# Performance work log

Hardware: AMD Instinct MI355X
Metric: run time of the kernel (lower is better)

## Reference

```python
import jax, jax.numpy as jnp
import numpy as np

B = 16384
INPUT_DIM = 2048
HIDDEN = 1536
N_COMP = 256
N_LAYERS = 32
TOP_K = 4


def setup_inputs() -> dict:
    key = jax.random.key(0)
    ks = jax.random.split(key, 12)
    s_in = 1.0 / np.sqrt(INPUT_DIM)
    s_h = 1.0 / np.sqrt(HIDDEN)
    s_3 = 1.0 / np.sqrt(3)
    return {
        "x": jax.random.normal(ks[0], (B, INPUT_DIM), dtype=jnp.float32),
        "layer_idx": 3,
        "embed": jax.random.normal(ks[1], (N_LAYERS, INPUT_DIM), dtype=jnp.float32),
        "enc_w1": jax.random.uniform(ks[2], (INPUT_DIM, HIDDEN), jnp.float32, -s_in, s_in),
        "enc_b1": jax.random.uniform(ks[3], (HIDDEN,), jnp.float32, -s_in, s_in),
        "enc_w2": jax.random.uniform(ks[4], (HIDDEN, N_COMP), jnp.float32, -s_h, s_h),
        "enc_b2": jax.random.uniform(ks[5], (N_COMP,), jnp.float32, -s_h, s_h),
        "components": jax.random.normal(ks[6], (N_COMP, 3), dtype=jnp.float32),
        "dec_w1": jax.random.uniform(ks[7], (3, HIDDEN), jnp.float32, -s_3, s_3),
        "dec_b1": jax.random.uniform(ks[8], (HIDDEN,), jnp.float32, -s_3, s_3),
        "dec_w2": jax.random.uniform(ks[9], (HIDDEN, INPUT_DIM), jnp.float32, -s_h, s_h),
        "dec_b2": jax.random.uniform(ks[10], (INPUT_DIM,), jnp.float32, -s_h, s_h),
    }


def reference(x, layer_idx, embed, enc_w1, enc_b1, enc_w2, enc_b2,
              components, dec_w1, dec_b1, dec_w2, dec_b2):
    # x: (B, D). Add per-layer embedding row.
    x = x + embed[layer_idx]
    # Encoder MLP: Linear -> GELU (exact, erf-based like torch default) -> Linear
    h = jax.nn.gelu(x @ enc_w1 + enc_b1, approximate=False)
    logits = h @ enc_w2 + enc_b2                     # (B, C)
    # Top-k gated masked softmax: softmax over only the top_k logits per row.
    vals, idx = jax.lax.top_k(logits, TOP_K)         # (B, K), (B, K)
    w = jax.nn.softmax(vals, axis=-1)                # (B, K)
    # Sparse mix: equivalent to masked_fill(-inf) softmax @ components
    pts = jnp.einsum('bk,bkc->bc', w, components[idx])  # (B, 3)
    # Decoder MLP
    d = jax.nn.gelu(pts @ dec_w1 + dec_b1, approximate=False)
    decoded = d @ dec_w2 + dec_b2                    # (B, D)
    encoded = jnp.broadcast_to(components[None], (x.shape[0], N_COMP, 3))
    return encoded, decoded
```

## Files before the change

### kernel.cpp

```cpp
#include <hip/hip_runtime.h>


typedef float  f32x4  __attribute__((ext_vector_type(4)));
typedef short  short8 __attribute__((ext_vector_type(8)));
typedef int    i32x4  __attribute__((ext_vector_type(4)));

#define DEVINL __device__ __forceinline__

constexpr int  NB      = 16384;
constexpr int  IN_DIM  = 2048;
constexpr int  HID     = 1536;
constexpr int  NC      = 256;
constexpr long ENC_ELEMS = (long)NB * NC * 3;
constexpr float TAU  = 2e-5f;
constexpr float TAU1 = 1.5e-3f;
constexpr int  MAXR  = 64;
constexpr int  M2CAP = 4096;
constexpr int  NKT1 = IN_DIM / 32;
constexpr int  NKT2 = HID / 32;

constexpr float SCALE_X  = 3251.2f;
constexpr float SCALE_W1 = 1471325.0f;
constexpr float SCALE_H  = 4644.5714f;
constexpr float SCALE_W2 = 1274205.0f;
constexpr double INV_S1 = 1.0 / ((double)SCALE_X * (double)SCALE_W1);
constexpr double INV_S2 = 1.0 / ((double)SCALE_H * (double)SCALE_W2);

DEVINL unsigned short f2bf(float f) {
  unsigned int u = __builtin_bit_cast(unsigned int, f);
  u = u + 0x7fffu + ((u >> 16) & 1u);
  return (unsigned short)(u >> 16);
}
DEVINL float bf2f(unsigned short h) {
  unsigned int u = ((unsigned int)h) << 16;
  return __builtin_bit_cast(float, u);
}
DEVINL float gelu_f(float v) {
  return 0.5f * v * (1.0f + erff(v * 0.70710678118654752440f));
}
DEVINL void llds16(const void* g, void* l) {
  __builtin_amdgcn_global_load_lds(
      (const __attribute__((address_space(1))) void*)g,
      (__attribute__((address_space(3))) void*)l, 16, 0, 0);
}
DEVINL f32x4 mfma_bf16(short8 a, short8 b, f32x4 c) {
  return __builtin_amdgcn_mfma_f32_16x16x32_bf16(a, b, c, 0, 0, 0);
}
DEVINL i32x4 mfma_i8(i32x4 a, i32x4 b, i32x4 c) {
  return __builtin_amdgcn_mfma_i32_16x16x64_i8(a, b, c, 0, 0, 0);
}
DEVINL long packed_off(long tileIdx, int rowp, int kq, int e) {
  int slot = kq ^ ((rowp >> 1) & 3);
  return (tileIdx * 512 + rowp * 4 + slot) * 8 + e;
}
DEVINL int swz_idx(int rowp, int kq) {
  return (rowp * 4 + (kq ^ ((rowp >> 1) & 3))) * 8;
}
DEVINL long i8_off(long tile64, int rowp, int kin64) {
  return tile64 * 8192 + rowp * 64 + kin64;
}
DEVINL int quant16(float v, float scale) {
  int q = (int)lrintf(v * scale);
  if (q >  32512) q =  32512;
  if (q < -32512) q = -32512;
  return q;
}

__global__ __launch_bounds__(256) void transpose_split_kernel(
    const float* __restrict__ in, int K, int N, int nkt,
    unsigned short* __restrict__ outH, unsigned short* __restrict__ outL)
{
  __shared__ float t[32][33];
  int tx = threadIdx.x & 31, ty = threadIdx.x >> 5;
  int n0 = blockIdx.x * 32, k0 = blockIdx.y * 32;
#pragma unroll
  for (int i = 0; i < 4; ++i)
    t[ty + i * 8][tx] = in[(long)(k0 + ty + i * 8) * N + n0 + tx];
  __syncthreads();

  int n = n0 + tx;
  int ntile = n >> 7, rowp = n & 127;
  int Kt = k0 >> 5;
  int j = ty & 3;
  long off = packed_off((long)ntile * nkt + Kt, rowp, j, 0);
  if (ty < 4) {
    short8 hv;
#pragma unroll
    for (int e = 0; e < 8; ++e) hv[e] = (short)f2bf(t[j * 8 + e][tx]);
    *(short8*)(outH + off) = hv;
  } else if (outL) {
    short8 lv;
#pragma unroll
    for (int e = 0; e < 8; ++e) {
      float f = t[j * 8 + e][tx];
      lv[e] = (short)f2bf(f - bf2f(f2bf(f)));
    }
    *(short8*)(outL + off) = lv;
  }
}

__global__ __launch_bounds__(256) void transpose_quant_kernel(
    const float* __restrict__ in, int K, int N, int nkt64, float scale,
    char* __restrict__ outH, char* __restrict__ outL)
{
  __shared__ float t[32][33];
  int tx = threadIdx.x & 31, ty = threadIdx.x >> 5;
  int n0 = blockIdx.x * 32, k0 = blockIdx.y * 32;
#pragma unroll
  for (int i = 0; i < 4; ++i)
    t[ty + i * 8][tx] = in[(long)(k0 + ty + i * 8) * N + n0 + tx];
  __syncthreads();

  int n = n0 + tx;
  int j = ty & 3;
  int kb = k0 + j * 8;
  long off = i8_off((long)(n >> 7) * nkt64 + (kb >> 6), n & 127, kb & 63);
  union { char b[8]; long v; } u;
  if (ty < 4) {
#pragma unroll
    for (int e = 0; e < 8; ++e) {
      int q = quant16(t[j * 8 + e][tx], scale);
      int lo = (q << 24) >> 24;
      u.b[e] = (char)((q - lo) >> 8);
    }
    *(long*)(outH + off) = u.v;
  } else {
#pragma unroll
    for (int e = 0; e < 8; ++e) {
      int q = quant16(t[j * 8 + e][tx], scale);
      u.b[e] = (char)((q << 24) >> 24);
    }
    *(long*)(outL + off) = u.v;
  }
}

__global__ __launch_bounds__(256) void quant_x_kernel(
    const float* __restrict__ x, const float* __restrict__ embedMat,
    const int* __restrict__ liPtr, char* __restrict__ Xh, char* __restrict__ Xl,
    int* __restrict__ cnt, int* __restrict__ cnt2)
{
  if (blockIdx.x == 0 && threadIdx.x == 0) { *cnt = 0; *cnt2 = 0; }
  long g = (long)blockIdx.x * 256 + threadIdx.x;
  int row = (int)(g >> 7);
  int k0 = ((int)(g & 127)) * 16;
  int li = liPtr[0];
  const float* xr = x + (long)row * IN_DIM + k0;
  const float* er = embedMat + (long)li * IN_DIM + k0;
  union { char b[16]; i32x4 v; } hu, lu;
#pragma unroll
  for (int c = 0; c < 4; ++c) {
    f32x4 a = *(const f32x4*)(xr + c * 4);
    f32x4 e = *(const f32x4*)(er + c * 4);
#pragma unroll
    for (int jj = 0; jj < 4; ++jj) {
      int q = quant16(a[jj] + e[jj], SCALE_X);
      int lo = (q << 24) >> 24;
      hu.b[c * 4 + jj] = (char)((q - lo) >> 8);
      lu.b[c * 4 + jj] = (char)lo;
    }
  }
  long off = i8_off((long)(row >> 7) * (IN_DIM / 64) + (k0 >> 6), row & 127, k0 & 63);
  *(i32x4*)(Xh + off) = hu.v;
  *(i32x4*)(Xl + off) = lu.v;
}

template<int OUT>
__global__ __launch_bounds__(256, 2) void gemm_i8_kernel(
    const char* __restrict__ Ah, const char* __restrict__ Al,
    const char* __restrict__ Bh, const char* __restrict__ Bl,
    int nkt64, const float* __restrict__ bias, double invScale,
    float* __restrict__ Cf, long ldc,
    char* __restrict__ Qh, char* __restrict__ Ql, int nktOut64, float outScale,
    int nbn)
{
  __shared__ alignas(16) char sAh[8192];
  __shared__ alignas(16) char sAl[8192];
  __shared__ alignas(16) char sBh[8192];
  __shared__ alignas(16) char sBl[8192];
  __shared__ float sBias[128];

  int tid = threadIdx.x;
  int nwg = gridDim.x, q = nwg >> 3, b0 = blockIdx.x;
  int sw = (b0 & 7) * q + (b0 >> 3);
  int bm = sw / nbn, bn = sw % nbn;

  if (tid < 128) sBias[tid] = bias[bn * 128 + tid];

  int wid = tid >> 6, lane = tid & 63;
  int wm = wid >> 1, wn = wid & 1;
  int l15 = lane & 15, kq = lane >> 4;

  i32x4 accH[4][4] = {};
  i32x4 accM[4][4] = {};

  for (int kt = 0; kt < nkt64; ++kt) {
    __syncthreads();
    {
      const char* g0 = Ah + ((long)(bm * nkt64 + kt)) * 8192 + tid * 16;
      llds16(g0, sAh + tid * 16); llds16(g0 + 4096, sAh + 4096 + tid * 16);
      const char* g1 = Al + ((long)(bm * nkt64 + kt)) * 8192 + tid * 16;
      llds16(g1, sAl + tid * 16); llds16(g1 + 4096, sAl + 4096 + tid * 16);
      const char* g2 = Bh + ((long)(bn * nkt64 + kt)) * 8192 + tid * 16;
      llds16(g2, sBh + tid * 16); llds16(g2 + 4096, sBh + 4096 + tid * 16);
      const char* g3 = Bl + ((long)(bn * nkt64 + kt)) * 8192 + tid * 16;
      llds16(g3, sBl + tid * 16); llds16(g3 + 4096, sBl + 4096 + tid * 16);
    }
    __syncthreads();

    i32x4 bhf[4], blf[4];
#pragma unroll
    for (int n = 0; n < 4; ++n) {
      int off = (wn * 64 + n * 16 + l15) * 64 + kq * 16;
      bhf[n] = *(const i32x4*)&sBh[off];
      blf[n] = *(const i32x4*)&sBl[off];
    }
#pragma unroll
    for (int m = 0; m < 4; ++m) {
      int off = (wm * 64 + m * 16 + l15) * 64 + kq * 16;
      i32x4 ahf = *(const i32x4*)&sAh[off];
      i32x4 alf = *(const i32x4*)&sAl[off];
#pragma unroll
      for (int n = 0; n < 4; ++n) {
        accH[m][n] = mfma_i8(ahf, bhf[n], accH[m][n]);
        accM[m][n] = mfma_i8(alf, bhf[n], accM[m][n]);
        accM[m][n] = mfma_i8(ahf, blf[n], accM[m][n]);
      }
    }
  }

#pragma unroll
  for (int m = 0; m < 4; ++m) {
#pragma unroll
    for (int n = 0; n < 4; ++n) {
      int  gcol = bn * 128 + wn * 64 + n * 16 + l15;
      float bb  = sBias[wn * 64 + n * 16 + l15];
#pragma unroll
      for (int r = 0; r < 4; ++r) {
        long grow = (long)bm * 128 + wm * 64 + m * 16 + kq * 4 + r;
        double dv = (double)accH[m][n][r] * 65536.0 + (double)accM[m][n][r] * 256.0;
        float v = (float)(dv * invScale) + bb;
        if constexpr (OUT == 0) {
          Cf[grow * ldc + gcol] = v;
        } else {
          v = gelu_f(v);
          int qq = quant16(v, outScale);
          int lo = (qq << 24) >> 24;
          long off = i8_off((long)(grow >> 7) * nktOut64 + (gcol >> 6),
                            (int)(grow & 127), gcol & 63);
          Qh[off] = (char)((qq - lo) >> 8);
          Ql[off] = (char)lo;
        }
      }
    }
  }
}

template<bool SPLIT, int OUT_MODE, bool GELU>
__global__ __launch_bounds__(256) void gemm2_kernel(
    const unsigned short* __restrict__ Ah, const unsigned short* __restrict__ Al,
    const unsigned short* __restrict__ Bh, const unsigned short* __restrict__ Bl,
    int nkt, const float* __restrict__ bias, float* __restrict__ Cf,
    unsigned short* __restrict__ Ch, unsigned short* __restrict__ Cl,
    long ldc, int nktOut, int nbn, const int* __restrict__ mrows, int mcap)
{
  __shared__ alignas(16) unsigned short sAh[4096];
  __shared__ alignas(16) unsigned short sAl[SPLIT ? 4096 : 8];
  __shared__ alignas(16) unsigned short sBh[4096];
  __shared__ alignas(16) unsigned short sBl[SPLIT ? 4096 : 8];
  __shared__ float sBias[128];

  int tid = threadIdx.x;
  int nwg = gridDim.x, q = nwg >> 3, b0 = blockIdx.x;
  int sw = (b0 & 7) * q + (b0 >> 3);
  int bm = sw / nbn, bn = sw % nbn;

  if (mrows) {
    int v = *mrows; if (v > mcap) v = mcap;
    if (bm * 128 >= v) return;
  }

  if (tid < 128) sBias[tid] = bias[bn * 128 + tid];

  int wid = tid >> 6, lane = tid & 63;
  int wm = wid >> 1, wn = wid & 1;
  int l15 = lane & 15, kq = lane >> 4;

  f32x4 acc[4][4] = {};

  for (int kt = 0; kt < nkt; ++kt) {
    __syncthreads();
    {
      const char* gA = (const char*)Ah + ((long)(bm * nkt + kt)) * 8192 + tid * 16;
      llds16(gA,        (char*)sAh + tid * 16);
      llds16(gA + 4096, (char*)sAh + 4096 + tid * 16);
    }
    if constexpr (SPLIT) {
      const char* gA = (const char*)Al + ((long)(bm * nkt + kt)) * 8192 + tid * 16;
      llds16(gA,        (char*)sAl + tid * 16);
      llds16(gA + 4096, (char*)sAl + 4096 + tid * 16);
    }
    {
      const char* gB = (const char*)Bh + ((long)(bn * nkt + kt)) * 8192 + tid * 16;
      llds16(gB,        (char*)sBh + tid * 16);
      llds16(gB + 4096, (char*)sBh + 4096 + tid * 16);
    }
    if constexpr (SPLIT) {
      const char* gB = (const char*)Bl + ((long)(bn * nkt + kt)) * 8192 + tid * 16;
      llds16(gB,        (char*)sBl + tid * 16);
      llds16(gB + 4096, (char*)sBl + 4096 + tid * 16);
    }
    __syncthreads();

    short8 bh[4], bl[4];
#pragma unroll
    for (int n = 0; n < 4; ++n) {
      int idx = swz_idx(wn * 64 + n * 16 + l15, kq);
      bh[n] = *(const short8*)&sBh[idx];
      if constexpr (SPLIT) bl[n] = *(const short8*)&sBl[idx];
    }
#pragma unroll
    for (int m = 0; m < 4; ++m) {
      int idx = swz_idx(wm * 64 + m * 16 + l15, kq);
      short8 ah = *(const short8*)&sAh[idx];
      short8 al;
      if constexpr (SPLIT) al = *(const short8*)&sAl[idx];
#pragma unroll
      for (int n = 0; n < 4; ++n) {
        acc[m][n] = mfma_bf16(ah, bh[n], acc[m][n]);
        if constexpr (SPLIT) {
          acc[m][n] = mfma_bf16(al, bh[n], acc[m][n]);
          acc[m][n] = mfma_bf16(ah, bl[n], acc[m][n]);
        }
      }
    }
  }

#pragma unroll
  for (int m = 0; m < 4; ++m) {
#pragma unroll
    for (int n = 0; n < 4; ++n) {
      int  gcol = bn * 128 + wn * 64 + n * 16 + l15;
      float bb  = sBias[wn * 64 + n * 16 + l15];
#pragma unroll
      for (int r = 0; r < 4; ++r) {
        long grow = (long)bm * 128 + wm * 64 + m * 16 + kq * 4 + r;
        float v = acc[m][n][r] + bb;
        if constexpr (GELU) v = gelu_f(v);
        if constexpr (OUT_MODE == 0) {
          Cf[grow * ldc + gcol] = v;
        } else {
          int Mt = (int)(grow >> 7), rowpo = (int)(grow & 127);
          int Kt = gcol >> 5, kqo = (gcol >> 3) & 3, e = gcol & 7;
          long off = packed_off((long)Mt * nktOut + Kt, rowpo, kqo, e);
          unsigned short hb = f2bf(v);
          Ch[off] = hb;
          Cl[off] = f2bf(v - bf2f(hb));
        }
      }
    }
  }
}

__global__ __launch_bounds__(256) void topk_screen_kernel(
    const float* __restrict__ logits, const float* __restrict__ comp,
    float* __restrict__ pts, float* __restrict__ encOut,
    int* __restrict__ cnt2, int* __restrict__ list2,
    int* __restrict__ rescueCnt, int* __restrict__ rescueList)
{
  int wid = threadIdx.x >> 6, lane = threadIdx.x & 63;
  long row = (long)blockIdx.x * 4 + wid;
  f32x4 v4 = *(const f32x4*)(logits + row * NC + lane * 4);
  float a[4] = {v4[0], v4[1], v4[2], v4[3]};

  float tv[5]; int ti[5];
#pragma unroll
  for (int t = 0; t < 5; ++t) {
    float lv = a[0]; int li = lane * 4;
#pragma unroll
    for (int i = 1; i < 4; ++i)
      if (a[i] > lv) { lv = a[i]; li = lane * 4 + i; }
#pragma unroll
    for (int off = 32; off >= 1; off >>= 1) {
      float ov = __shfl_xor(lv, off);
      int   oi = __shfl_xor(li, off);
      if (ov > lv || (ov == lv && oi < li)) { lv = ov; li = oi; }
    }
    tv[t] = lv; ti[t] = li;
    if (t < 4 && (li >> 2) == lane) a[li & 3] = -INFINITY;
  }

  bool flag = (tv[3] - tv[4]) < TAU1;
  if (!flag) {
    float m = tv[0], w[4], s = 0.f;
#pragma unroll
    for (int t = 0; t < 4; ++t) { w[t] = expf(tv[t] - m); s += w[t]; }
    float inv = 1.0f / s;
    if (lane < 3) {
      float p = 0.f;
#pragma unroll
      for (int t = 0; t < 4; ++t) p += w[t] * inv * comp[ti[t] * 3 + lane];
      pts[row * 3 + lane] = p;
    }
  } else if (lane == 0) {
    int pos = atomicAdd(cnt2, 1);
    if (pos < M2CAP) list2[pos] = (int)row;
    else { int rp = atomicAdd(rescueCnt, 1); rescueList[rp] = (int)row; }
  }

  long base = (long)blockIdx.x * 3072;
  for (int j = threadIdx.x; j < 3072; j += 256)
    encOut[base + j] = comp[j % 768];
}

__global__ __launch_bounds__(256) void gather_kernel(
    const float* __restrict__ x, const float* __restrict__ embedMat,
    const int* __restrict__ liPtr, const int* __restrict__ cnt2,
    const int* __restrict__ list2,
    unsigned short* __restrict__ A2h, unsigned short* __restrict__ A2l)
{
  int i = blockIdx.x;
  int c2 = *cnt2; if (c2 > M2CAP) c2 = M2CAP;
  if (i >= c2) return;
  int row = list2[i];
  int li = liPtr[0];
  int t = threadIdx.x;
  int k0 = t * 8;
  const float* xr = x + (long)row * IN_DIM + k0;
  const float* er = embedMat + (long)li * IN_DIM + k0;
  short8 hv, lv;
#pragma unroll
  for (int c = 0; c < 2; ++c) {
    f32x4 a = *(const f32x4*)(xr + c * 4);
    f32x4 e = *(const f32x4*)(er + c * 4);
#pragma unroll
    for (int jj = 0; jj < 4; ++jj) {
      float f = a[jj] + e[jj];
      unsigned short hb = f2bf(f);
      hv[c * 4 + jj] = (short)hb;
      lv[c * 4 + jj] = (short)f2bf(f - bf2f(hb));
    }
  }
  long off = packed_off((long)(i >> 7) * NKT1 + (k0 >> 5), i & 127, (k0 >> 3) & 3, 0);
  *(short8*)(A2h + off) = hv;
  *(short8*)(A2l + off) = lv;
}

__global__ __launch_bounds__(256) void topk_final_kernel(
    const float* __restrict__ logits2, const float* __restrict__ comp,
    const int* __restrict__ cnt2, const int* __restrict__ list2,
    float* __restrict__ pts, int* __restrict__ rescueCnt, int* __restrict__ rescueList)
{
  int wid = threadIdx.x >> 6, lane = threadIdx.x & 63;
  int slot = blockIdx.x * 4 + wid;
  int c2 = *cnt2; if (c2 > M2CAP) c2 = M2CAP;
  if (slot >= c2) return;
  int row = list2[slot];
  f32x4 v4 = *(const f32x4*)(logits2 + (long)slot * NC + lane * 4);
  float a[4] = {v4[0], v4[1], v4[2], v4[3]};

  float tv[5]; int ti[5];
#pragma unroll
  for (int t = 0; t < 5; ++t) {
    float lv = a[0]; int li = lane * 4;
#pragma unroll
    for (int i = 1; i < 4; ++i)
      if (a[i] > lv) { lv = a[i]; li = lane * 4 + i; }
#pragma unroll
    for (int off = 32; off >= 1; off >>= 1) {
      float ov = __shfl_xor(lv, off);
      int   oi = __shfl_xor(li, off);
      if (ov > lv || (ov == lv && oi < li)) { lv = ov; li = oi; }
    }
    tv[t] = lv; ti[t] = li;
    if (t < 4 && (li >> 2) == lane) a[li & 3] = -INFINITY;
  }

  float m = tv[0], w[4], s = 0.f;
#pragma unroll
  for (int t = 0; t < 4; ++t) { w[t] = expf(tv[t] - m); s += w[t]; }
  float inv = 1.0f / s;
  if (lane < 3) {
    float p = 0.f;
#pragma unroll
    for (int t = 0; t < 4; ++t) p += w[t] * inv * comp[ti[t] * 3 + lane];
    pts[(long)row * 3 + lane] = p;
  }
  if (lane == 0 && (tv[3] - tv[4]) < TAU) {
    int pos = atomicAdd(rescueCnt, 1);
    rescueList[pos] = row;
  }
}

__global__ __launch_bounds__(256) void rescue_h1_kernel(
    const float* __restrict__ x, const float* __restrict__ embedMat,
    const int* __restrict__ liPtr, const float* __restrict__ W1,
    const int* __restrict__ cnt, const int* __restrict__ list,
    double* __restrict__ partial)
{
  int b = blockIdx.x;
  int s = b / 24, rem = b % 24;
  int cc = rem >> 2, kp = rem & 3;
  int n = *cnt;
  if (s >= n || s >= MAXR) return;
  int row = list[s];
  __shared__ double xd[512];
  int tid = threadIdx.x;
  int li = liPtr[0];
  int k0 = kp * 512;
  for (int j = tid; j < 512; j += 256)
    xd[j] = (double)x[(long)row * IN_DIM + k0 + j]
          + (double)embedMat[(long)li * IN_DIM + k0 + j];
  __syncthreads();
  int c = cc * 256 + tid;
  const float* wp = W1 + (long)k0 * HID + c;
  double s0 = 0, s1 = 0, s2 = 0, s3 = 0;
  for (int k = 0; k < 512; k += 4) {
    s0 += xd[k]     * (double)wp[(long)k * HID];
    s1 += xd[k + 1] * (double)wp[(long)(k + 1) * HID];
    s2 += xd[k + 2] * (double)wp[(long)(k + 2) * HID];
    s3 += xd[k + 3] * (double)wp[(long)(k + 3) * HID];
  }
  partial[((long)(s * 6 + cc) * 4 + kp) * 256 + tid] = (s0 + s1) + (s2 + s3);
}

__global__ __launch_bounds__(256) void rescue_h2_kernel(
    const float* __restrict__ b1, const int* __restrict__ cnt,
    const double* __restrict__ partial, double* __restrict__ hbuf)
{
  int b = blockIdx.x;
  int s = b / 6, cc = b % 6;
  int n = *cnt;
  if (s >= n || s >= MAXR) return;
  int tid = threadIdx.x;
  long base = ((long)(s * 6 + cc) * 4) * 256 + tid;
  double v = (double)b1[cc * 256 + tid]
           + ((partial[base] + partial[base + 256])
            + (partial[base + 512] + partial[base + 768]));
  hbuf[(long)s * HID + cc * 256 + tid]
      = 0.5 * v * (1.0 + erf(v * 0.70710678118654752440));
}

__global__ __launch_bounds__(256) void rescue_logits_kernel(
    const float* __restrict__ W2, const float* __restrict__ b2,
    const float* __restrict__ comp, const int* __restrict__ cnt,
    const int* __restrict__ list, const double* __restrict__ hbuf,
    float* __restrict__ pts)
{
  int s = blockIdx.x;
  int n = *cnt;
  if (s >= n || s >= MAXR) return;
  __shared__ double hd[HID];
  __shared__ double ld[NC];
  int tid = threadIdx.x;
  for (int j = tid; j < HID; j += 256) hd[j] = hbuf[(long)s * HID + j];
  __syncthreads();
  {
    const float* wp = W2 + tid;
    double a0 = 0, a1 = 0, a2 = 0, a3 = 0;
    for (int k = 0; k < HID; k += 4) {
      a0 += hd[k]     * (double)wp[(long)k * NC];
      a1 += hd[k + 1] * (double)wp[(long)(k + 1) * NC];
      a2 += hd[k + 2] * (double)wp[(long)(k + 2) * NC];
      a3 += hd[k + 3] * (double)wp[(long)(k + 3) * NC];
    }
    ld[tid] = (double)b2[tid] + ((a0 + a1) + (a2 + a3));
  }
  __syncthreads();
  if (tid == 0) {
    int row = list[s];
    int idx[4]; double val[4];
    unsigned long long mask[4] = {0, 0, 0, 0};
    for (int t = 0; t < 4; ++t) {
      double bv = -1e300; int bi = 0;
      for (int j = 0; j < NC; ++j) {
        if ((mask[j >> 6] >> (j & 63)) & 1ull) continue;
        if (ld[j] > bv) { bv = ld[j]; bi = j; }
      }
      idx[t] = bi; val[t] = bv; mask[bi >> 6] |= 1ull << (bi & 63);
    }
    double m = val[0], w[4], sum = 0;
    for (int t = 0; t < 4; ++t) { w[t] = exp(val[t] - m); sum += w[t]; }
    for (int c = 0; c < 3; ++c) {
      double p = 0;
      for (int t = 0; t < 4; ++t) p += (w[t] / sum) * (double)comp[idx[t] * 3 + c];
      pts[(long)row * 3 + c] = (float)p;
    }
  }
}

__global__ __launch_bounds__(256) void rescue_slow_kernel(
    const float* __restrict__ x, const float* __restrict__ embedMat,
    const int* __restrict__ liPtr, const float* __restrict__ W1,
    const float* __restrict__ b1, const float* __restrict__ W2,
    const float* __restrict__ b2, const float* __restrict__ comp,
    float* __restrict__ pts, const int* __restrict__ cnt, const int* __restrict__ list)
{
  __shared__ double xd[IN_DIM];
  __shared__ double hd[HID];
  __shared__ double ld[NC];
  int tid = threadIdx.x;
  int li = liPtr[0];
  int n = *cnt;
  for (int it = MAXR + blockIdx.x; it < n; it += gridDim.x) {
    int row = list[it];
    const float* xr = x + (long)row * IN_DIM;
    const float* er = embedMat + (long)li * IN_DIM;
    for (int j = tid; j < IN_DIM; j += 256)
      xd[j] = (double)xr[j] + (double)er[j];
    __syncthreads();
    for (int c = tid; c < HID; c += 256) {
      double s0 = 0, s1 = 0, s2 = 0, s3 = 0;
      const float* wp = W1 + c;
      for (int k = 0; k < IN_DIM; k += 4) {
        s0 += xd[k]     * (double)wp[(long)k * HID];
        s1 += xd[k + 1] * (double)wp[(long)(k + 1) * HID];
        s2 += xd[k + 2] * (double)wp[(long)(k + 2) * HID];
        s3 += xd[k + 3] * (double)wp[(long)(k + 3) * HID];
      }
      double s = (double)b1[c] + ((s0 + s1) + (s2 + s3));
      hd[c] = 0.5 * s * (1.0 + erf(s * 0.70710678118654752440));
    }
    __syncthreads();
    {
      int c = tid;
      double s0 = 0, s1 = 0, s2 = 0, s3 = 0;
      const float* wp = W2 + c;
      for (int k = 0; k < HID; k += 4) {
        s0 += hd[k]     * (double)wp[(long)k * NC];
        s1 += hd[k + 1] * (double)wp[(long)(k + 1) * NC];
        s2 += hd[k + 2] * (double)wp[(long)(k + 2) * NC];
        s3 += hd[k + 3] * (double)wp[(long)(k + 3) * NC];
      }
      ld[c] = (double)b2[c] + ((s0 + s1) + (s2 + s3));
    }
    __syncthreads();
    if (tid == 0) {
      int idx[4]; double val[4];
      unsigned long long mask[4] = {0, 0, 0, 0};
      for (int t = 0; t < 4; ++t) {
        double bv = -1e300; int bi = 0;
        for (int j = 0; j < NC; ++j) {
          if ((mask[j >> 6] >> (j & 63)) & 1ull) continue;
          if (ld[j] > bv) { bv = ld[j]; bi = j; }
        }
        idx[t] = bi; val[t] = bv; mask[bi >> 6] |= 1ull << (bi & 63);
      }
      double m = val[0], w[4], s = 0;
      for (int t = 0; t < 4; ++t) { w[t] = exp(val[t] - m); s += w[t]; }
      for (int c = 0; c < 3; ++c) {
        double p = 0;
        for (int t = 0; t < 4; ++t) p += (w[t] / s) * (double)comp[idx[t] * 3 + c];
        pts[(long)row * 3 + c] = (float)p;
      }
    }
    __syncthreads();
  }
}

__global__ __launch_bounds__(256) void dec_a_kernel(
    const float* __restrict__ pts, const float* __restrict__ W1d,
    const float* __restrict__ b1d, unsigned short* __restrict__ dout)
{
  int  j = (blockIdx.x % 6) * 256 + threadIdx.x;
  long b = blockIdx.x / 6;
  const float* p = pts + b * 3;
  float s = fmaf(p[0], W1d[j], fmaf(p[1], W1d[HID + j], fmaf(p[2], W1d[2 * HID + j], b1d[j])));
  int Mt = (int)(b >> 7), rowp = (int)(b & 127);
  int Kt = j >> 5, kq = (j >> 3) & 3, e = j & 7;
  dout[packed_off((long)Mt * NKT2 + Kt, rowp, kq, e)] = f2bf(gelu_f(s));
}

extern "C" void kernel_launch(void* const* d_in, const int* in_sizes, int n_in,
                              void* d_out, int out_size, void* d_ws, size_t ws_size,
                              hipStream_t stream) {
  const float* x     = (const float*)d_in[0];
  const int*   liPtr = (const int*)  d_in[1];
  const float* embed = (const float*)d_in[2];
  const float* W1    = (const float*)d_in[3];
  const float* b1    = (const float*)d_in[4];
  const float* W2    = (const float*)d_in[5];
  const float* b2    = (const float*)d_in[6];
  const float* comp  = (const float*)d_in[7];
  const float* W1d   = (const float*)d_in[8];
  const float* b1d   = (const float*)d_in[9];
  const float* W2d   = (const float*)d_in[10];
  const float* b2d   = (const float*)d_in[11];
  float* out = (float*)d_out;

  char* w = (char*)d_ws;
  unsigned short* W1hT = (unsigned short*)(w);
  unsigned short* W1lT = (unsigned short*)(w + 6291456);
  unsigned short* W2hT = (unsigned short*)(w + 12582912);
  unsigned short* W2lT = (unsigned short*)(w + 13369344);
  unsigned short* W2dT = (unsigned short*)(w + 14155776);
  char* W1qh = w + 20447232;
  char* W1ql = w + 23592960;
  char* W2qh = w + 26738688;
  char* W2ql = w + 27131904;
  char* Xqh = w + 27525120;
  char* Xql = w + 61079552;
  char* Hqh = w + 94633984;
  char* Hql = w + 119799808;
  float* logits = (float*)(w + 144965632);
  unsigned short* A2h = (unsigned short*)(w + 161742848);
  unsigned short* A2l = (unsigned short*)(w + 178520064);
  unsigned short* H2h = (unsigned short*)(w + 195297280);
  unsigned short* H2l = (unsigned short*)(w + 207880192);
  float* logits2 = (float*)(w + 220463104);
  unsigned short* dbuf = (unsigned short*)(w + 27525120);
  float* pts   = (float*)(w + 224657408);
  int*   cnt   = (int*)  (w + 224854016);
  int*   cnt2  = (int*)  (w + 224854272);
  int*   list  = (int*)  (w + 224854528);
  int*   list2 = (int*)  (w + 224920064);
  double* partial = (double*)(w + 224936448);
  double* hbuf    = (double*)(w + 228082176);

  transpose_split_kernel<<<dim3(HID / 32, IN_DIM / 32), 256, 0, stream>>>(W1, IN_DIM, HID, NKT1, W1hT, W1lT);
  transpose_split_kernel<<<dim3(NC / 32, HID / 32),     256, 0, stream>>>(W2, HID, NC, NKT2, W2hT, W2lT);
  transpose_split_kernel<<<dim3(IN_DIM / 32, HID / 32), 256, 0, stream>>>(W2d, HID, IN_DIM, NKT2, W2dT, nullptr);
  transpose_quant_kernel<<<dim3(HID / 32, IN_DIM / 32), 256, 0, stream>>>(W1, IN_DIM, HID, IN_DIM / 64, SCALE_W1, W1qh, W1ql);
  transpose_quant_kernel<<<dim3(NC / 32, HID / 32),     256, 0, stream>>>(W2, HID, NC, HID / 64, SCALE_W2, W2qh, W2ql);

  quant_x_kernel<<<NB * 128 / 256, 256, 0, stream>>>(x, embed, liPtr, Xqh, Xql, cnt, cnt2);
  gemm_i8_kernel<1><<<(NB / 128) * (HID / 128), 256, 0, stream>>>(
      Xqh, Xql, W1qh, W1ql, IN_DIM / 64, b1, INV_S1,
      nullptr, 0, Hqh, Hql, HID / 64, SCALE_H, HID / 128);
  gemm_i8_kernel<0><<<(NB / 128) * (NC / 128), 256, 0, stream>>>(
      Hqh, Hql, W2qh, W2ql, HID / 64, b2, INV_S2,
      logits, NC, nullptr, nullptr, 0, 0.f, NC / 128);

  topk_screen_kernel<<<NB / 4, 256, 0, stream>>>(logits, comp, pts, out, cnt2, list2, cnt, list);

  gather_kernel<<<M2CAP, 256, 0, stream>>>(x, embed, liPtr, cnt2, list2, A2h, A2l);
  gemm2_kernel<true, 2, true><<<(M2CAP / 128) * (HID / 128), 256, 0, stream>>>(
      A2h, A2l, W1hT, W1lT, NKT1, b1, nullptr, H2h, H2l, 0, NKT2, HID / 128, cnt2, M2CAP);
  gemm2_kernel<true, 0, false><<<(M2CAP / 128) * (NC / 128), 256, 0, stream>>>(
      H2h, H2l, W2hT, W2lT, NKT2, b2, logits2, nullptr, nullptr, NC, 0, NC / 128, cnt2, M2CAP);
  topk_final_kernel<<<M2CAP / 4, 256, 0, stream>>>(logits2, comp, cnt2, list2, pts, cnt, list);

  rescue_h1_kernel<<<MAXR * 24, 256, 0, stream>>>(x, embed, liPtr, W1, cnt, list, partial);
  rescue_h2_kernel<<<MAXR * 6,  256, 0, stream>>>(b1, cnt, partial, hbuf);
  rescue_logits_kernel<<<MAXR,  256, 0, stream>>>(W2, b2, comp, cnt, list, hbuf, pts);
  rescue_slow_kernel<<<64, 256, 0, stream>>>(x, embed, liPtr, W1, b1, W2, b2, comp, pts, cnt, list);

  dec_a_kernel<<<NB * (HID / 256), 256, 0, stream>>>(pts, W1d, b1d, dbuf);
  gemm2_kernel<false, 0, false><<<(NB / 128) * (IN_DIM / 128), 256, 0, stream>>>(
      dbuf, nullptr, W2dT, nullptr, NKT2, b2d, out + ENC_ELEMS, nullptr, nullptr,
      IN_DIM, 0, IN_DIM / 128, nullptr, 0);
}
```

Measured before the change: 753.0 us.

## Halve recompute cap, unroll K in split GEMMs, vectorize encOut, grid-stride dec_a

Four separate changes. The cap on rows sent to the precise recompute path drops from 4096 to 2048, and the split-bf16 recompute GEMMs now stage four K tiles per barrier pair instead of one. The broadcast of components into the encoded output uses 16-byte vector stores, and the decoder first layer uses a fixed 3072-block grid-stride loop instead of one block per 256 outputs. Fewer barriers and launches are the aim, but the larger shared-memory footprint (about 128KB for the split GEMM) cuts occupancy, and a smaller cap pushes more overflow rows onto the slow rescue path.

```diff
diff --git a/kernel.cpp b/kernel.cpp
--- a/kernel.cpp
+++ b/kernel.cpp
@@ -15,7 +15,7 @@
 constexpr float TAU  = 2e-5f;
 constexpr float TAU1 = 1.5e-3f;
 constexpr int  MAXR  = 64;
-constexpr int  M2CAP = 4096;
+constexpr int  M2CAP = 2048;
 constexpr int  NKT1 = IN_DIM / 32;
 constexpr int  NKT2 = HID / 32;
 
@@ -255,7 +255,7 @@
   }
 }
 
-template<bool SPLIT, int OUT_MODE, bool GELU>
+template<bool SPLIT, int OUT_MODE, bool GELU, int KU>
 __global__ __launch_bounds__(256) void gemm2_kernel(
     const unsigned short* __restrict__ Ah, const unsigned short* __restrict__ Al,
     const unsigned short* __restrict__ Bh, const unsigned short* __restrict__ Bl,
@@ -263,10 +263,10 @@
     unsigned short* __restrict__ Ch, unsigned short* __restrict__ Cl,
     long ldc, int nktOut, int nbn, const int* __restrict__ mrows, int mcap)
 {
-  __shared__ alignas(16) unsigned short sAh[4096];
-  __shared__ alignas(16) unsigned short sAl[SPLIT ? 4096 : 8];
-  __shared__ alignas(16) unsigned short sBh[4096];
-  __shared__ alignas(16) unsigned short sBl[SPLIT ? 4096 : 8];
+  __shared__ alignas(16) unsigned short sAh[4096 * KU];
+  __shared__ alignas(16) unsigned short sAl[SPLIT ? 4096 * KU : 8];
+  __shared__ alignas(16) unsigned short sBh[4096 * KU];
+  __shared__ alignas(16) unsigned short sBl[SPLIT ? 4096 * KU : 8];
   __shared__ float sBias[128];
 
   int tid = threadIdx.x;
@@ -287,49 +287,55 @@
 
   f32x4 acc[4][4] = {};
 
-  for (int kt = 0; kt < nkt; ++kt) {
+  for (int kt = 0; kt < nkt; kt += KU) {
     __syncthreads();
-    {
-      const char* gA = (const char*)Ah + ((long)(bm * nkt + kt)) * 8192 + tid * 16;
-      llds16(gA,        (char*)sAh + tid * 16);
-      llds16(gA + 4096, (char*)sAh + 4096 + tid * 16);
-    }
-    if constexpr (SPLIT) {
-      const char* gA = (const char*)Al + ((long)(bm * nkt + kt)) * 8192 + tid * 16;
-      llds16(gA,        (char*)sAl + tid * 16);
-      llds16(gA + 4096, (char*)sAl + 4096 + tid * 16);
-    }
-    {
-      const char* gB = (const char*)Bh + ((long)(bn * nkt + kt)) * 8192 + tid * 16;
-      llds16(gB,        (char*)sBh + tid * 16);
-      llds16(gB + 4096, (char*)sBh + 4096 + tid * 16);
-    }
-    if constexpr (SPLIT) {
-      const char* gB = (const char*)Bl + ((long)(bn * nkt + kt)) * 8192 + tid * 16;
-      llds16(gB,        (char*)sBl + tid * 16);
-      llds16(gB + 4096, (char*)sBl + 4096 + tid * 16);
+#pragma unroll
+    for (int u = 0; u < KU; ++u) {
+      {
+        const char* gA = (const char*)Ah + ((long)(bm * nkt + kt + u)) * 8192 + tid * 16;
+        llds16(gA,        (char*)sAh + u * 8192 + tid * 16);
+        llds16(gA + 4096, (char*)sAh + u * 8192 + 4096 + tid * 16);
+      }
+      if constexpr (SPLIT) {
+        const char* gA = (const char*)Al + ((long)(bm * nkt + kt + u)) * 8192 + tid * 16;
+        llds16(gA,        (char*)sAl + u * 8192 + tid * 16);
+        llds16(gA + 4096, (char*)sAl + u * 8192 + 4096 + tid * 16);
+      }
+      {
+        const char* gB = (const char*)Bh + ((long)(bn * nkt + kt + u)) * 8192 + tid * 16;
+        llds16(gB,        (char*)sBh + u * 8192 + tid * 16);
+        llds16(gB + 4096, (char*)sBh + u * 8192 + 4096 + tid * 16);
+      }
+      if constexpr (SPLIT) {
+        const char* gB = (const char*)Bl + ((long)(bn * nkt + kt + u)) * 8192 + tid * 16;
+        llds16(gB,        (char*)sBl + u * 8192 + tid * 16);
+        llds16(gB + 4096, (char*)sBl + u * 8192 + 4096 + tid * 16);
+      }
     }
     __syncthreads();
 
-    short8 bh[4], bl[4];
-#pragma unroll
-    for (int n = 0; n < 4; ++n) {
-      int idx = swz_idx(wn * 64 + n * 16 + l15, kq);
-      bh[n] = *(const short8*)&sBh[idx];
-      if constexpr (SPLIT) bl[n] = *(const short8*)&sBl[idx];
-    }
-#pragma unroll
-    for (int m = 0; m < 4; ++m) {
-      int idx = swz_idx(wm * 64 + m * 16 + l15, kq);
-      short8 ah = *(const short8*)&sAh[idx];
-      short8 al;
-      if constexpr (SPLIT) al = *(const short8*)&sAl[idx];
+#pragma unroll
+    for (int u = 0; u < KU; ++u) {
+      short8 bh[4], bl[4];
 #pragma unroll
       for (int n = 0; n < 4; ++n) {
-        acc[m][n] = mfma_bf16(ah, bh[n], acc[m][n]);
-        if constexpr (SPLIT) {
-          acc[m][n] = mfma_bf16(al, bh[n], acc[m][n]);
-          acc[m][n] = mfma_bf16(ah, bl[n], acc[m][n]);
+        int idx = u * 4096 + swz_idx(wn * 64 + n * 16 + l15, kq);
+        bh[n] = *(const short8*)&sBh[idx];
+        if constexpr (SPLIT) bl[n] = *(const short8*)&sBl[idx];
+      }
+#pragma unroll
+      for (int m = 0; m < 4; ++m) {
+        int idx = u * 4096 + swz_idx(wm * 64 + m * 16 + l15, kq);
+        short8 ah = *(const short8*)&sAh[idx];
+        short8 al;
+        if constexpr (SPLIT) al = *(const short8*)&sAl[idx];
+#pragma unroll
+        for (int n = 0; n < 4; ++n) {
+          acc[m][n] = mfma_bf16(ah, bh[n], acc[m][n]);
+          if constexpr (SPLIT) {
+            acc[m][n] = mfma_bf16(al, bh[n], acc[m][n]);
+            acc[m][n] = mfma_bf16(ah, bl[n], acc[m][n]);
+          }
         }
       }
     }
@@ -407,9 +413,10 @@
     else { int rp = atomicAdd(rescueCnt, 1); rescueList[rp] = (int)row; }
   }
 
-  long base = (long)blockIdx.x * 3072;
-  for (int j = threadIdx.x; j < 3072; j += 256)
-    encOut[base + j] = comp[j % 768];
+  const f32x4* cv = (const f32x4*)comp;
+  f32x4* ov = (f32x4*)encOut + (long)blockIdx.x * 768;
+  for (int j = threadIdx.x; j < 768; j += 256)
+    ov[j] = cv[j % 192];
 }
 
 __global__ __launch_bounds__(256) void gather_kernel(
@@ -661,13 +668,15 @@
     const float* __restrict__ pts, const float* __restrict__ W1d,
     const float* __restrict__ b1d, unsigned short* __restrict__ dout)
 {
-  int  j = (blockIdx.x % 6) * 256 + threadIdx.x;
-  long b = blockIdx.x / 6;
-  const float* p = pts + b * 3;
-  float s = fmaf(p[0], W1d[j], fmaf(p[1], W1d[HID + j], fmaf(p[2], W1d[2 * HID + j], b1d[j])));
-  int Mt = (int)(b >> 7), rowp = (int)(b & 127);
-  int Kt = j >> 5, kq = (j >> 3) & 3, e = j & 7;
-  dout[packed_off((long)Mt * NKT2 + Kt, rowp, kq, e)] = f2bf(gelu_f(s));
+  for (long u = blockIdx.x; u < (long)NB * 6; u += gridDim.x) {
+    int  j = (int)(u % 6) * 256 + threadIdx.x;
+    long b = u / 6;
+    const float* p = pts + b * 3;
+    float s = fmaf(p[0], W1d[j], fmaf(p[1], W1d[HID + j], fmaf(p[2], W1d[2 * HID + j], b1d[j])));
+    int Mt = (int)(b >> 7), rowp = (int)(b & 127);
+    int Kt = j >> 5, kq = (j >> 3) & 3, e = j & 7;
+    dout[packed_off((long)Mt * NKT2 + Kt, rowp, kq, e)] = f2bf(gelu_f(s));
+  }
 }
 
 extern "C" void kernel_launch(void* const* d_in, const int* in_sizes, int n_in,
@@ -733,9 +742,9 @@
   topk_screen_kernel<<<NB / 4, 256, 0, stream>>>(logits, comp, pts, out, cnt2, list2, cnt, list);
 
   gather_kernel<<<M2CAP, 256, 0, stream>>>(x, embed, liPtr, cnt2, list2, A2h, A2l);
-  gemm2_kernel<true, 2, true><<<(M2CAP / 128) * (HID / 128), 256, 0, stream>>>(
+  gemm2_kernel<true, 2, true, 4><<<(M2CAP / 128) * (HID / 128), 256, 0, stream>>>(
       A2h, A2l, W1hT, W1lT, NKT1, b1, nullptr, H2h, H2l, 0, NKT2, HID / 128, cnt2, M2CAP);
-  gemm2_kernel<true, 0, false><<<(M2CAP / 128) * (NC / 128), 256, 0, stream>>>(
+  gemm2_kernel<true, 0, false, 4><<<(M2CAP / 128) * (NC / 128), 256, 0, stream>>>(
       H2h, H2l, W2hT, W2lT, NKT2, b2, logits2, nullptr, nullptr, NC, 0, NC / 128, cnt2, M2CAP);
   topk_final_kernel<<<M2CAP / 4, 256, 0, stream>>>(logits2, comp, cnt2, list2, pts, cnt, list);
 
@@ -744,8 +753,8 @@
   rescue_logits_kernel<<<MAXR,  256, 0, stream>>>(W2, b2, comp, cnt, list, hbuf, pts);
   rescue_slow_kernel<<<64, 256, 0, stream>>>(x, embed, liPtr, W1, b1, W2, b2, comp, pts, cnt, list);
 
-  dec_a_kernel<<<NB * (HID / 256), 256, 0, stream>>>(pts, W1d, b1d, dbuf);
-  gemm2_kernel<false, 0, false><<<(NB / 128) * (IN_DIM / 128), 256, 0, stream>>>(
+  dec_a_kernel<<<3072, 256, 0, stream>>>(pts, W1d, b1d, dbuf);
+  gemm2_kernel<false, 0, false, 1><<<(NB / 128) * (IN_DIM / 128), 256, 0, stream>>>(
       dbuf, nullptr, W2dT, nullptr, NKT2, b2d, out + ENC_ELEMS, nullptr, nullptr,
       IN_DIM, 0, IN_DIM / 128, nullptr, 0);
 }
```

New measurement: 743.5 us. About the same (-1.3%).
